# Performance work log

Measured on AMD Instinct MI355X. Metric: run time of the kernel, lower is better.

The kernel has to match this reference:

```python
import jax, jax.numpy as jnp
import numpy as np

HEADS = 8
DIM_HEAD = 64
KNN = 32
SCALE = DIM_HEAD ** -0.5


def setup_inputs() -> dict:
    key = jax.random.key(0)
    k1, k2, k3 = jax.random.split(key, 3)
    B, N, C = 2, 2048, 256
    inner = HEADS * DIM_HEAD  # 512
    x = jax.random.normal(k1, (B, N, C), dtype=jnp.float32)
    Wqkv = jax.random.normal(k2, (C, 3 * inner), dtype=jnp.float32) * (C ** -0.5)
    Wout = jax.random.normal(k3, (inner, C), dtype=jnp.float32) * (inner ** -0.5)
    bout = jnp.zeros((C,), dtype=jnp.float32)
    return {"x": x, "Wqkv": Wqkv, "Wout": Wout, "bout": bout}


def _knn_adjacency(x, k):
    # x: [B, N, C] -> boolean adjacency [B, N, N], k nearest neighbors by
    # euclidean distance, self-loops excluded (loop=False).
    B, N, _ = x.shape
    x2 = jnp.sum(x * x, axis=-1)  # [B, N]
    # squared distances [B, N, N]
    d2 = x2[:, :, None] + x2[:, None, :] - 2.0 * jnp.einsum('bnc,bmc->bnm', x, x)
    big = jnp.finfo(d2.dtype).max
    d2 = d2 + big * jnp.eye(N, dtype=d2.dtype)  # exclude self
    _, idx = jax.lax.top_k(-d2, k)  # [B, N, k] nearest neighbor indices

    rows = jnp.arange(N)[:, None]  # [N, 1]

    def scatter_one(idx_b):
        return jnp.zeros((N, N), dtype=bool).at[rows, idx_b].set(True)

    return jax.vmap(scatter_one)(idx)  # [B, N, N]


def reference(x, Wqkv, Wout, bout):
    B, N, C = x.shape
    adj = _knn_adjacency(x, KNN)  # [B, N, N] bool, shared across heads

    qkv = x @ Wqkv  # [B, N, 3*inner]
    q, k, v = jnp.split(qkv, 3, axis=-1)
    split_heads = lambda t: t.reshape(B, N, HEADS, DIM_HEAD).transpose(0, 2, 1, 3)
    q, k, v = split_heads(q), split_heads(k), split_heads(v)  # [B, H, N, d]

    dots = jnp.einsum('bhnd,bhmd->bhnm', q, k) * SCALE  # [B, H, N, N]
    dots = jnp.where(adj[:, None, :, :], dots, -jnp.inf)
    attn = jax.nn.softmax(dots, axis=-1)
    out = jnp.einsum('bhnm,bhmd->bhnd', attn, v)  # [B, H, N, d]
    out = out.transpose(0, 2, 1, 3).reshape(B, N, HEADS * DIM_HEAD)
    return out @ Wout + bout
```

## Files before the change

kernel.cpp:

```cpp
#include <hip/hip_runtime.h>
#include <hip/hip_bf16.h>
#include <hip/hip_fp16.h>

#define BATCH 2
#define NPTS  2048
#define CDIM  256
#define NHEAD 8
#define DHEAD 64
#define INNER 512
#define TRIPLE 1536
#define KNN   32
#define SCALE 0.125f

typedef __attribute__((ext_vector_type(8))) short short8;
typedef __attribute__((ext_vector_type(4))) float floatx4;
typedef __attribute__((ext_vector_type(4))) unsigned short ushort4v;
typedef unsigned short ushort;

#define TW  32
#define TSZ (128*TW)

__device__ __forceinline__ unsigned bfsplit(float x) {
    unsigned u = __float_as_uint(x);
    unsigned r = u + 0x7fffu + ((u >> 16) & 1u);
    unsigned hs = r >> 16;
    float hf = __uint_as_float(hs << 16);
    float lo = x - hf;
    unsigned u2 = __float_as_uint(lo);
    unsigned r2 = u2 + 0x7fffu + ((u2 >> 16) & 1u);
    return (hs & 0xffffu) | (r2 & 0xffff0000u);
}

__device__ __forceinline__ void bfsplit3(float x, ushort* hh, ushort* ll, ushort* qq) {
    unsigned u = __float_as_uint(x);
    unsigned r = u + 0x7fffu + ((u >> 16) & 1u);
    unsigned hs = r >> 16;
    float hf = __uint_as_float(hs << 16);
    float d1 = x - hf;
    unsigned u2 = __float_as_uint(d1);
    unsigned r2 = u2 + 0x7fffu + ((u2 >> 16) & 1u);
    unsigned ls = r2 >> 16;
    float lf = __uint_as_float(ls << 16);
    float d2 = d1 - lf;
    unsigned u3 = __float_as_uint(d2);
    unsigned r3 = u3 + 0x7fffu + ((u3 >> 16) & 1u);
    *hh = (ushort)hs;
    *ll = (ushort)ls;
    *qq = (ushort)(r3 >> 16);
}

__device__ __forceinline__ ushort f2h(float f) {
    __half h = __float2half(f);
    return *reinterpret_cast<ushort*>(&h);
}
__device__ __forceinline__ float h2f(ushort u) {
    __half h;
    *reinterpret_cast<ushort*>(&h) = u;
    return __half2float(h);
}

__global__ __launch_bounds__(256) void input_prep_kernel(const float* __restrict__ x,
                                                         float* __restrict__ x2,
                                                         ushort* __restrict__ xhi,
                                                         ushort* __restrict__ xlo,
                                                         ushort* __restrict__ xqd) {
    int wave = threadIdx.x >> 6, lane = threadIdx.x & 63;
    int row = blockIdx.x * 4 + wave;
    const float* xr = x + (size_t)row * CDIM;
    float4 v = *(const float4*)(xr + lane * 4);
    float s = v.x*v.x + v.y*v.y + v.z*v.z + v.w*v.w;
    #pragma unroll
    for (int o = 32; o; o >>= 1) s += __shfl_down(s, o);
    if (lane == 0) x2[row] = s;

    ushort h[4], l[4], q[4];
    bfsplit3(v.x, &h[0], &l[0], &q[0]);
    bfsplit3(v.y, &h[1], &l[1], &q[1]);
    bfsplit3(v.z, &h[2], &l[2], &q[2]);
    bfsplit3(v.w, &h[3], &l[3], &q[3]);
    size_t off = (size_t)row * CDIM + lane * 4;
    *(ushort4v*)(xhi + off) = *(ushort4v*)h;
    *(ushort4v*)(xlo + off) = *(ushort4v*)l;
    *(ushort4v*)(xqd + off) = *(ushort4v*)q;
}

__global__ __launch_bounds__(256) void wtrans2_kernel(const float* __restrict__ Wqkv,
                                                      const float* __restrict__ Wout,
                                                      ushort* __restrict__ wqhiT,
                                                      ushort* __restrict__ wqloT,
                                                      ushort* __restrict__ wohiT,
                                                      ushort* __restrict__ woloT) {
    __shared__ float tile[64][65];
    const float* W; ushort* hiT; ushort* loT; int K, N, bx, by;
    int bid = blockIdx.x;
    if (bid < 96) { W = Wqkv; hiT = wqhiT; loT = wqloT; K = CDIM;  N = TRIPLE; bx = bid % 24; by = bid / 24; }
    else { int t = bid - 96; W = Wout; hiT = wohiT; loT = woloT; K = INNER; N = CDIM;  bx = t % 4;  by = t / 4; }
    int k0 = by * 64, n0 = bx * 64;
    #pragma unroll
    for (int i = 0; i < 4; ++i) {
        int f = threadIdx.x + i * 256;
        int r = f >> 4, c4 = (f & 15) * 4;
        float4 v = *(const float4*)(W + (size_t)(k0 + r) * N + n0 + c4);
        tile[r][c4+0] = v.x; tile[r][c4+1] = v.y;
        tile[r][c4+2] = v.z; tile[r][c4+3] = v.w;
    }
    __syncthreads();
    #pragma unroll
    for (int i = 0; i < 4; ++i) {
        int f = threadIdx.x + i * 256;
        int rn = f >> 4, ck = (f & 15) * 4;
        unsigned p0 = bfsplit(tile[ck+0][rn]);
        unsigned p1 = bfsplit(tile[ck+1][rn]);
        unsigned p2 = bfsplit(tile[ck+2][rn]);
        unsigned p3 = bfsplit(tile[ck+3][rn]);
        ushort4v h, l;
        h.x = (ushort)p0; l.x = (ushort)(p0 >> 16);
        h.y = (ushort)p1; l.y = (ushort)(p1 >> 16);
        h.z = (ushort)p2; l.z = (ushort)(p2 >> 16);
        h.w = (ushort)p3; l.w = (ushort)(p3 >> 16);
        *(ushort4v*)(hiT + (size_t)(n0 + rn) * K + k0 + ck) = h;
        *(ushort4v*)(loT + (size_t)(n0 + rn) * K + k0 + ck) = l;
    }
}


__device__ __forceinline__ void gemm_split_body(const ushort* __restrict__ Ahi,
                                                const ushort* __restrict__ Alo,
                                                const ushort* __restrict__ BhiT,
                                                const ushort* __restrict__ BloT,
                                                const float* __restrict__ bias,
                                                float* __restrict__ C,
                                                int N, int K, int bi, int bj,
                                                ushort* lds,
                                                ushort* __restrict__ kv16) {
    int lane = threadIdx.x & 63, wave = threadIdx.x >> 6;
    int wr = wave >> 1, wc = wave & 1;
    int fr = lane & 15, kg = lane >> 4;
    int swz8 = (kg ^ ((fr >> 1) & 3)) * 8;

    int srow = threadIdx.x >> 1;
    int hc = (threadIdx.x & 1) * 2;
    int sw = (srow >> 1) & 3;
    int d0 = srow * TW + ((hc + 0) ^ sw) * 8;
    int d1 = srow * TW + ((hc + 1) ^ sw) * 8;

    const ushort* g0 = Ahi  + (size_t)(bi + srow) * K + hc * 8;
    const ushort* g1 = Alo  + (size_t)(bi + srow) * K + hc * 8;
    const ushort* g2 = BhiT + (size_t)(bj + srow) * K + hc * 8;
    const ushort* g3 = BloT + (size_t)(bj + srow) * K + hc * 8;

    floatx4 acc[4][4] = {};

    for (int k0 = 0; k0 < K; k0 += 32) {
        uint4 va0 = *(const uint4*)(g0 + k0);
        uint4 va1 = *(const uint4*)(g0 + k0 + 8);
        uint4 vb0 = *(const uint4*)(g1 + k0);
        uint4 vb1 = *(const uint4*)(g1 + k0 + 8);
        uint4 vc0 = *(const uint4*)(g2 + k0);
        uint4 vc1 = *(const uint4*)(g2 + k0 + 8);
        uint4 vd0 = *(const uint4*)(g3 + k0);
        uint4 vd1 = *(const uint4*)(g3 + k0 + 8);
        *(uint4*)&lds[0*TSZ + d0] = va0;  *(uint4*)&lds[0*TSZ + d1] = va1;
        *(uint4*)&lds[1*TSZ + d0] = vb0;  *(uint4*)&lds[1*TSZ + d1] = vb1;
        *(uint4*)&lds[2*TSZ + d0] = vc0;  *(uint4*)&lds[2*TSZ + d1] = vc1;
        *(uint4*)&lds[3*TSZ + d0] = vd0;  *(uint4*)&lds[3*TSZ + d1] = vd1;
        __syncthreads();

        short8 a_h[4], a_l[4], b_h[4], b_l[4];
        #pragma unroll
        for (int m = 0; m < 4; ++m) {
            int off = (wr*64 + m*16 + fr) * TW + swz8;
            a_h[m] = *(const short8*)&lds[0*TSZ + off];
            a_l[m] = *(const short8*)&lds[1*TSZ + off];
        }
        #pragma unroll
        for (int n = 0; n < 4; ++n) {
            int off = (wc*64 + n*16 + fr) * TW + swz8;
            b_h[n] = *(const short8*)&lds[2*TSZ + off];
            b_l[n] = *(const short8*)&lds[3*TSZ + off];
        }
        #pragma unroll
        for (int m = 0; m < 4; ++m)
            #pragma unroll
            for (int n = 0; n < 4; ++n) {
                acc[m][n] = __builtin_amdgcn_mfma_f32_16x16x32_bf16(a_h[m], b_h[n], acc[m][n], 0, 0, 0);
                acc[m][n] = __builtin_amdgcn_mfma_f32_16x16x32_bf16(a_h[m], b_l[n], acc[m][n], 0, 0, 0);
                acc[m][n] = __builtin_amdgcn_mfma_f32_16x16x32_bf16(a_l[m], b_h[n], acc[m][n], 0, 0, 0);
            }
        __syncthreads();
    }

    #pragma unroll
    for (int m = 0; m < 4; ++m)
        #pragma unroll
        for (int n = 0; n < 4; ++n) {
            int col = bj + wc*64 + n*16 + fr;
            float bv = bias ? bias[col] : 0.0f;
            #pragma unroll
            for (int r = 0; r < 4; ++r) {
                int row = bi + wr*64 + m*16 + kg*4 + r;
                float val = acc[m][n][r] + bv;
                C[(size_t)row * N + col] = val;
                if (kv16 && col >= INNER)
                    kv16[(size_t)row * 1024 + (col - INNER)] = f2h(val);
            }
        }
}

__device__ __forceinline__ void gram_body(const ushort* __restrict__ Ah,
                                          const ushort* __restrict__ Al,
                                          const ushort* __restrict__ Aq,
                                          const float* __restrict__ x2b,
                                          float* __restrict__ Sb,
                                          int bi, int bj, ushort* lds) {
    int lane = threadIdx.x & 63, wave = threadIdx.x >> 6;
    int wr = wave >> 1, wc = wave & 1;
    int fr = lane & 15, kg = lane >> 4;
    int swz8 = (kg ^ ((fr >> 1) & 3)) * 8;

    int srow = threadIdx.x >> 1;
    int hc = (threadIdx.x & 1) * 2;
    int sw = (srow >> 1) & 3;
    int d0 = srow * TW + ((hc + 0) ^ sw) * 8;
    int d1 = srow * TW + ((hc + 1) ^ sw) * 8;

    const ushort* g0 = Ah + (size_t)(bi + srow) * CDIM + hc * 8;
    const ushort* g1 = Al + (size_t)(bi + srow) * CDIM + hc * 8;
    const ushort* g2 = Aq + (size_t)(bi + srow) * CDIM + hc * 8;
    const ushort* g3 = Ah + (size_t)(bj + srow) * CDIM + hc * 8;
    const ushort* g4 = Al + (size_t)(bj + srow) * CDIM + hc * 8;
    const ushort* g5 = Aq + (size_t)(bj + srow) * CDIM + hc * 8;

    floatx4 acc[4][4] = {};

    for (int k0 = 0; k0 < CDIM; k0 += 32) {
        uint4 a0 = *(const uint4*)(g0 + k0); uint4 a1 = *(const uint4*)(g0 + k0 + 8);
        uint4 b0 = *(const uint4*)(g1 + k0); uint4 b1 = *(const uint4*)(g1 + k0 + 8);
        uint4 c0 = *(const uint4*)(g2 + k0); uint4 c1 = *(const uint4*)(g2 + k0 + 8);
        uint4 e0 = *(const uint4*)(g3 + k0); uint4 e1 = *(const uint4*)(g3 + k0 + 8);
        uint4 f0 = *(const uint4*)(g4 + k0); uint4 f1 = *(const uint4*)(g4 + k0 + 8);
        uint4 h0 = *(const uint4*)(g5 + k0); uint4 h1 = *(const uint4*)(g5 + k0 + 8);
        *(uint4*)&lds[0*TSZ + d0] = a0; *(uint4*)&lds[0*TSZ + d1] = a1;
        *(uint4*)&lds[1*TSZ + d0] = b0; *(uint4*)&lds[1*TSZ + d1] = b1;
        *(uint4*)&lds[2*TSZ + d0] = c0; *(uint4*)&lds[2*TSZ + d1] = c1;
        *(uint4*)&lds[3*TSZ + d0] = e0; *(uint4*)&lds[3*TSZ + d1] = e1;
        *(uint4*)&lds[4*TSZ + d0] = f0; *(uint4*)&lds[4*TSZ + d1] = f1;
        *(uint4*)&lds[5*TSZ + d0] = h0; *(uint4*)&lds[5*TSZ + d1] = h1;
        __syncthreads();

        short8 a_h[4], a_l[4], a_q[4], b_h[4], b_l[4], b_q[4];
        #pragma unroll
        for (int m = 0; m < 4; ++m) {
            int off = (wr*64 + m*16 + fr) * TW + swz8;
            a_h[m] = *(const short8*)&lds[0*TSZ + off];
            a_l[m] = *(const short8*)&lds[1*TSZ + off];
            a_q[m] = *(const short8*)&lds[2*TSZ + off];
        }
        #pragma unroll
        for (int n = 0; n < 4; ++n) {
            int off = (wc*64 + n*16 + fr) * TW + swz8;
            b_h[n] = *(const short8*)&lds[3*TSZ + off];
            b_l[n] = *(const short8*)&lds[4*TSZ + off];
            b_q[n] = *(const short8*)&lds[5*TSZ + off];
        }
        #pragma unroll
        for (int m = 0; m < 4; ++m)
            #pragma unroll
            for (int n = 0; n < 4; ++n) {
                acc[m][n] = __builtin_amdgcn_mfma_f32_16x16x32_bf16(a_h[m], b_h[n], acc[m][n], 0, 0, 0);
                acc[m][n] = __builtin_amdgcn_mfma_f32_16x16x32_bf16(a_h[m], b_l[n], acc[m][n], 0, 0, 0);
                acc[m][n] = __builtin_amdgcn_mfma_f32_16x16x32_bf16(a_l[m], b_h[n], acc[m][n], 0, 0, 0);
                acc[m][n] = __builtin_amdgcn_mfma_f32_16x16x32_bf16(a_l[m], b_l[n], acc[m][n], 0, 0, 0);
                acc[m][n] = __builtin_amdgcn_mfma_f32_16x16x32_bf16(a_h[m], b_q[n], acc[m][n], 0, 0, 0);
                acc[m][n] = __builtin_amdgcn_mfma_f32_16x16x32_bf16(a_q[m], b_h[n], acc[m][n], 0, 0, 0);
            }
        __syncthreads();
    }

    #pragma unroll
    for (int m = 0; m < 4; ++m)
        #pragma unroll
        for (int n = 0; n < 4; ++n) {
            int col = bj + wc*64 + n*16 + fr;
            float xc = x2b[col];
            #pragma unroll
            for (int r = 0; r < 4; ++r) {
                int row = bi + wr*64 + m*16 + kg*4 + r;
                float val = xc - 2.0f * acc[m][n][r];
                if (row == col) val = __builtin_inff();
                Sb[(size_t)row * NPTS + col] = val;
            }
        }

    if (bi != bj) {
        float* T = (float*)lds;
        #pragma unroll
        for (int p = 0; p < 2; ++p) {
            __syncthreads();
            if (wc == p) {
                #pragma unroll
                for (int m = 0; m < 4; ++m) {
                    int row0 = wr*64 + m*16 + kg*4;
                    float x0 = x2b[bi + row0 + 0];
                    float x1 = x2b[bi + row0 + 1];
                    float x2v = x2b[bi + row0 + 2];
                    float x3 = x2b[bi + row0 + 3];
                    #pragma unroll
                    for (int n = 0; n < 4; ++n) {
                        int colp = n*16 + fr;
                        float4 v;
                        v.x = x0 - 2.0f * acc[m][n][0];
                        v.y = x1 - 2.0f * acc[m][n][1];
                        v.z = x2v - 2.0f * acc[m][n][2];
                        v.w = x3 - 2.0f * acc[m][n][3];
                        *(float4*)&T[colp * 132 + row0] = v;
                    }
                }
            }
            __syncthreads();
            #pragma unroll
            for (int i = 0; i < 8; ++i) {
                int f = threadIdx.x + i * 256;
                int cr = f >> 5, c4 = (f & 31) * 4;
                float4 v = *(const float4*)&T[cr * 132 + c4];
                *(float4*)(Sb + (size_t)(bj + p*64 + cr) * NPTS + bi + c4) = v;
            }
        }
    }
}

__global__ __launch_bounds__(256) void fused_mfma_kernel(const ushort* __restrict__ xh,
                                                         const ushort* __restrict__ xl,
                                                         const ushort* __restrict__ xq,
                                                         const float* __restrict__ x2,
                                                         float* __restrict__ S,
                                                         const ushort* __restrict__ wqhiT,
                                                         const ushort* __restrict__ wqloT,
                                                         float* __restrict__ qkv,
                                                         ushort* __restrict__ kv16) {
    __shared__ ushort lds[6*TSZ];
    int bid = blockIdx.x;
    if (bid < 272) {
        int b = bid / 136, t = bid % 136;
        int by = 0;
        while (t >= 16 - by) { t -= 16 - by; ++by; }
        int bx = by + t;
        size_t xoff = (size_t)b * NPTS * CDIM;
        gram_body(xh + xoff, xl + xoff, xq + xoff,
                  x2 + (size_t)b * NPTS, S + (size_t)b * NPTS * NPTS,
                  by * 128, bx * 128, lds);
    } else {
        int t = bid - 272;
        int bx = t % 12, by = t / 12;
        gemm_split_body(xh, xl, wqhiT, wqloT, nullptr, qkv,
                        TRIPLE, CDIM, by * 128, bx * 128, lds, kv16);
    }
}

__global__ __launch_bounds__(256) void outproj_kernel(const ushort* __restrict__ Ahi,
                                                      const ushort* __restrict__ Alo,
                                                      const ushort* __restrict__ BhiT,
                                                      const ushort* __restrict__ BloT,
                                                      const float* __restrict__ bias,
                                                      float* __restrict__ C) {
    __shared__ ushort lds[4*TSZ];
    gemm_split_body(Ahi, Alo, BhiT, BloT, bias, C,
                    CDIM, INNER, blockIdx.y * 128, blockIdx.x * 128, lds, nullptr);
}

__device__ __forceinline__ unsigned block_excl_scan_256(unsigned c,
                                                        unsigned* wsum,
                                                        unsigned* total_out) {
    unsigned v = c;
    #pragma unroll
    for (int o = 1; o < 64; o <<= 1) {
        unsigned t = __shfl_up(v, o);
        if ((threadIdx.x & 63) >= o) v += t;
    }
    if ((threadIdx.x & 63) == 63) wsum[threadIdx.x >> 6] = v;
    __syncthreads();
    unsigned woff = 0;
    int mywave = threadIdx.x >> 6;
    #pragma unroll
    for (int w = 0; w < 4; ++w) {
        unsigned s = wsum[w];
        if (w < mywave) woff += s;
    }
    if (total_out) *total_out = wsum[0] + wsum[1] + wsum[2] + wsum[3];
    __syncthreads();
    return v + woff - c;
}

__global__ __launch_bounds__(256) void knn_attn_kernel(const float* __restrict__ S,
                                                       const float* __restrict__ qkv,
                                                       const ushort* __restrict__ kv16,
                                                       ushort* __restrict__ ahi,
                                                       ushort* __restrict__ alo) {
    int bid = blockIdx.x;
    int b = (bid & 7) >> 2;
    int n = ((bid >> 3) << 2) | (bid & 3);
    size_t rowoff = (size_t)b * NPTS + n;
    const float* row = S + rowoff * NPTS;

    __shared__ unsigned keys[NPTS];
    __shared__ unsigned hist[256];
    __shared__ unsigned wsum[4];
    __shared__ unsigned s_red[8];
    __shared__ unsigned sh_lo, sh_hi, sh_rank, sh_cnt, sh_break;
    __shared__ unsigned ckey[64];
    __shared__ int     cidx[64];
    __shared__ unsigned s_ccount;
    __shared__ int   nb[KNN];
    __shared__ float dots[NHEAD][KNN];
    __shared__ float p[NHEAD][KNN];

    int tid = threadIdx.x;

    unsigned mn = 0xffffffffu, mx = 0u;
    {
        int i0 = tid * 8;
        float4 f0 = *(const float4*)(row + i0);
        float4 f1 = *(const float4*)(row + i0 + 4);
        float fv[8] = { f0.x, f0.y, f0.z, f0.w, f1.x, f1.y, f1.z, f1.w };
        #pragma unroll
        for (int t = 0; t < 8; ++t) {
            int i = i0 + t;
            unsigned u;
            if (i == n) {
                u = 0xffffffffu;
            } else {
                unsigned v = __float_as_uint(fv[t]);
                u = (v & 0x80000000u) ? ~v : (v | 0x80000000u);
                mn = min(mn, u); mx = max(mx, u);
            }
            keys[i] = u;
        }
    }
    #pragma unroll
    for (int o = 32; o; o >>= 1) {
        mn = min(mn, (unsigned)__shfl_xor((int)mn, o));
        mx = max(mx, (unsigned)__shfl_xor((int)mx, o));
    }
    if ((tid & 63) == 0) { s_red[tid >> 6] = mn; s_red[4 + (tid >> 6)] = mx; }
    __syncthreads();
    if (tid == 0) {
        unsigned a = min(min(s_red[0], s_red[1]), min(s_red[2], s_red[3]));
        unsigned z = max(max(s_red[4], s_red[5]), max(s_red[6], s_red[7]));
        sh_lo = a; sh_hi = z; sh_rank = KNN; sh_break = 0; s_ccount = 0;
    }
    __syncthreads();

    for (int it = 0; it < 5; ++it) {
        unsigned lo = sh_lo, hi = sh_hi;
        unsigned range1 = hi - lo;
        int shift = 0;
        if (range1 > 255u) shift = 24 - __clz(range1);
        hist[tid] = 0;
        __syncthreads();
        for (int i = tid; i < NPTS; i += 256) {
            unsigned u = keys[i];
            if (u >= lo && u <= hi)
                atomicAdd(&hist[(u - lo) >> shift], 1u);
        }
        __syncthreads();
        unsigned c = hist[tid];
        unsigned rank = sh_rank;
        unsigned excl = block_excl_scan_256(c, wsum, nullptr);
        if (excl < rank && excl + c >= rank) {
            sh_rank = rank - excl;
            unsigned nlo = lo + ((unsigned)tid << shift);
            unsigned span = (shift == 0) ? 0u : (((1u << shift)) - 1u);
            unsigned nhi = nlo + span;
            if (nhi > hi || nhi < nlo) nhi = hi;
            sh_lo = nlo; sh_hi = nhi;
            sh_cnt = c;
            sh_break = (shift == 0 || c <= 64u) ? 1u : 0u;
        }
        __syncthreads();
        if (sh_break) break;
    }

    unsigned lo = sh_lo, hi = sh_hi, rank = sh_rank, cnt = sh_cnt;

    unsigned lt = 0;
    for (int i = tid; i < NPTS; i += 256) lt += (keys[i] < lo) ? 1u : 0u;
    unsigned pos = block_excl_scan_256(lt, wsum, nullptr);
    for (int i = tid; i < NPTS; i += 256) {
        unsigned u = keys[i];
        if (u < lo) nb[pos++] = i;
        else if (u >= lo && u <= hi && cnt <= 64u) {
            unsigned pp = atomicAdd(&s_ccount, 1u);
            ckey[pp] = u; cidx[pp] = i;
        }
    }
    __syncthreads();

    unsigned base = KNN - rank;
    if (cnt <= 64u) {
        if (tid < (int)cnt) {
            unsigned myk = ckey[tid]; int myi = cidx[tid];
            unsigned r = 0;
            for (unsigned s = 0; s < cnt; ++s) {
                unsigned sk = ckey[s]; int si = cidx[s];
                r += (sk < myk || (sk == myk && si < myi)) ? 1u : 0u;
            }
            if (r < rank) nb[base + r] = myi;
        }
    } else {
        if (tid == 0) {
            unsigned need = rank, pp = base;
            for (int i = 0; i < NPTS && need; ++i) {
                if (keys[i] >= lo && keys[i] <= hi) { nb[pp++] = i; --need; }
            }
        }
    }
    __syncthreads();

    const float* qrow = qkv + rowoff * TRIPLE;
    const ushort* kvb = kv16 + (size_t)b * NPTS * 1024;

    {
        int j = tid >> 3;
        int l = tid & 7;
        const ushort* krow = kvb + (size_t)nb[j] * 1024 + l * 8;
        short8 kr[NHEAD];
        #pragma unroll
        for (int h = 0; h < NHEAD; ++h)
            kr[h] = *(const short8*)(krow + h * DHEAD);
        const float* qp = qrow + l * 8;
        #pragma unroll
        for (int h = 0; h < NHEAD; ++h) {
            float4 q0 = *(const float4*)(qp + h * DHEAD);
            float4 q1 = *(const float4*)(qp + h * DHEAD + 4);
            float d = h2f((ushort)kr[h][0]) * q0.x + h2f((ushort)kr[h][1]) * q0.y
                    + h2f((ushort)kr[h][2]) * q0.z + h2f((ushort)kr[h][3]) * q0.w
                    + h2f((ushort)kr[h][4]) * q1.x + h2f((ushort)kr[h][5]) * q1.y
                    + h2f((ushort)kr[h][6]) * q1.z + h2f((ushort)kr[h][7]) * q1.w;
            d += __shfl_xor(d, 1);
            d += __shfl_xor(d, 2);
            d += __shfl_xor(d, 4);
            if (l == 0) dots[h][j] = d * SCALE;
        }
    }
    __syncthreads();

    {
        int h = tid >> 5, jj = tid & 31;
        float dv = dots[h][jj];
        float mxv = dv;
        for (int o = 16; o; o >>= 1) mxv = fmaxf(mxv, __shfl_xor(mxv, o));
        float e = expf(dv - mxv);
        float s = e;
        for (int o = 16; o; o >>= 1) s += __shfl_xor(s, o);
        p[h][jj] = e / s;
    }
    __syncthreads();

    {
        int hd = tid >> 5;
        int jd = tid & 31;
        const ushort* vb = kvb + INNER + hd * DHEAD + jd * 2;
        float o0 = 0.f, o1 = 0.f;
        #pragma unroll
        for (int g = 0; g < 4; ++g) {
            unsigned vv[8]; float pw[8];
            #pragma unroll
            for (int t = 0; t < 8; ++t) {
                int jj = g * 8 + t;
                vv[t] = *(const unsigned*)(vb + (size_t)nb[jj] * 1024);
                pw[t] = p[hd][jj];
            }
            #pragma unroll
            for (int t = 0; t < 8; ++t) {
                o0 += pw[t] * h2f((ushort)(vv[t] & 0xffffu));
                o1 += pw[t] * h2f((ushort)(vv[t] >> 16));
            }
        }
        size_t baseo = rowoff * INNER + hd * DHEAD + jd * 2;
        unsigned q0 = bfsplit(o0);
        unsigned q1 = bfsplit(o1);
        *(unsigned*)(ahi + baseo) = (q0 & 0xffffu) | (q1 << 16);
        *(unsigned*)(alo + baseo) = (q0 >> 16) | (q1 & 0xffff0000u);
    }
}

extern "C" void kernel_launch(void* const* d_in, const int* in_sizes, int n_in,
                              void* d_out, int out_size, void* d_ws, size_t ws_size,
                              hipStream_t stream) {
    const float* x    = (const float*)d_in[0];
    const float* Wqkv = (const float*)d_in[1];
    const float* Wout = (const float*)d_in[2];
    const float* bout = (const float*)d_in[3];
    float* out = (float*)d_out;

    float* S    = (float*)d_ws;
    float* x2   = S + (size_t)BATCH * NPTS * NPTS;
    float* qkv  = x2 + (size_t)BATCH * NPTS;
    ushort* kv16 = (ushort*)(qkv + (size_t)BATCH * NPTS * TRIPLE);
    ushort* xhi = kv16 + (size_t)BATCH * NPTS * 1024;
    ushort* xlo   = xhi   + (size_t)BATCH * NPTS * CDIM;
    ushort* xqd   = xlo   + (size_t)BATCH * NPTS * CDIM;
    ushort* ahi   = xqd   + (size_t)BATCH * NPTS * CDIM;
    ushort* alo   = ahi   + (size_t)BATCH * NPTS * INNER;
    ushort* wqhiT = alo   + (size_t)BATCH * NPTS * INNER;
    ushort* wqloT = wqhiT + (size_t)TRIPLE * CDIM;
    ushort* wohiT = wqloT + (size_t)TRIPLE * CDIM;
    ushort* woloT = wohiT + (size_t)CDIM * INNER;

    input_prep_kernel<<<(BATCH * NPTS) / 4, 256, 0, stream>>>(x, x2, xhi, xlo, xqd);

    wtrans2_kernel<<<128, 256, 0, stream>>>(Wqkv, Wout, wqhiT, wqloT, wohiT, woloT);

    fused_mfma_kernel<<<656, 256, 0, stream>>>(xhi, xlo, xqd, x2, S,
                                               wqhiT, wqloT, qkv, kv16);

    knn_attn_kernel<<<BATCH * NPTS, 256, 0, stream>>>(S, qkv, kv16, ahi, alo);

    {
        dim3 grid(CDIM / 128, (BATCH * NPTS) / 128);
        outproj_kernel<<<grid, 256, 0, stream>>>(ahi, alo, wohiT, woloT, bout, out);
    }
}
```

Before: 109.0 us.

## Use atomic work queue in fused GEMM kernel and drop redundant fp32 K/V stores

Replaces the static block-to-tile mapping in the fused Gram/QKV kernel with a persistent-style loop: blocks pull items from a global atomic counter that the input-prep kernel resets. Gram tiles are handed out first and QKV tiles after, which is meant to improve load balance. The QKV epilogue now writes only Q in fp32, into a compact [rows,512] buffer, and K/V only as fp16. This removes the redundant fp32 K/V stores and their memory traffic. The cost is an atomic plus two block barriers per item, and a 768-block grid that oversubscribes the 656 items.

```diff
diff --git a/kernel.cpp b/kernel.cpp
--- a/kernel.cpp
+++ b/kernel.cpp
@@ -11,6 +11,10 @@
 #define TRIPLE 1536
 #define KNN   32
 #define SCALE 0.125f
+
+#define GRAM_ITEMS 272
+#define QKV_ITEMS  384
+#define TOTAL_ITEMS (GRAM_ITEMS + QKV_ITEMS)
 
 typedef __attribute__((ext_vector_type(8))) short short8;
 typedef __attribute__((ext_vector_type(4))) float floatx4;
@@ -63,7 +67,9 @@
                                                          float* __restrict__ x2,
                                                          ushort* __restrict__ xhi,
                                                          ushort* __restrict__ xlo,
-                                                         ushort* __restrict__ xqd) {
+                                                         ushort* __restrict__ xqd,
+                                                         unsigned* __restrict__ wq) {
+    if (blockIdx.x == 0 && threadIdx.x == 0) *wq = 0u;
     int wave = threadIdx.x >> 6, lane = threadIdx.x & 63;
     int row = blockIdx.x * 4 + wave;
     const float* xr = x + (size_t)row * CDIM;
@@ -190,21 +196,35 @@
         __syncthreads();
     }
 
-    #pragma unroll
-    for (int m = 0; m < 4; ++m)
-        #pragma unroll
-        for (int n = 0; n < 4; ++n) {
-            int col = bj + wc*64 + n*16 + fr;
-            float bv = bias ? bias[col] : 0.0f;
-            #pragma unroll
-            for (int r = 0; r < 4; ++r) {
-                int row = bi + wr*64 + m*16 + kg*4 + r;
-                float val = acc[m][n][r] + bv;
-                C[(size_t)row * N + col] = val;
-                if (kv16 && col >= INNER)
-                    kv16[(size_t)row * 1024 + (col - INNER)] = f2h(val);
-            }
-        }
+    if (kv16) {
+        bool is_q = (bj < INNER);
+        #pragma unroll
+        for (int m = 0; m < 4; ++m)
+            #pragma unroll
+            for (int n = 0; n < 4; ++n) {
+                int col = bj + wc*64 + n*16 + fr;
+                #pragma unroll
+                for (int r = 0; r < 4; ++r) {
+                    int row = bi + wr*64 + m*16 + kg*4 + r;
+                    float val = acc[m][n][r];
+                    if (is_q) C[(size_t)row * INNER + col] = val;
+                    else      kv16[(size_t)row * 1024 + (col - INNER)] = f2h(val);
+                }
+            }
+    } else {
+        #pragma unroll
+        for (int m = 0; m < 4; ++m)
+            #pragma unroll
+            for (int n = 0; n < 4; ++n) {
+                int col = bj + wc*64 + n*16 + fr;
+                float bv = bias ? bias[col] : 0.0f;
+                #pragma unroll
+                for (int r = 0; r < 4; ++r) {
+                    int row = bi + wr*64 + m*16 + kg*4 + r;
+                    C[(size_t)row * N + col] = acc[m][n][r] + bv;
+                }
+            }
+    }
 }
 
 __device__ __forceinline__ void gram_body(const ushort* __restrict__ Ah,
@@ -336,24 +356,32 @@
                                                          float* __restrict__ S,
                                                          const ushort* __restrict__ wqhiT,
                                                          const ushort* __restrict__ wqloT,
-                                                         float* __restrict__ qkv,
-                                                         ushort* __restrict__ kv16) {
+                                                         float* __restrict__ q,
+                                                         ushort* __restrict__ kv16,
+                                                         unsigned* __restrict__ wq) {
     __shared__ ushort lds[6*TSZ];
-    int bid = blockIdx.x;
-    if (bid < 272) {
-        int b = bid / 136, t = bid % 136;
-        int by = 0;
-        while (t >= 16 - by) { t -= 16 - by; ++by; }
-        int bx = by + t;
-        size_t xoff = (size_t)b * NPTS * CDIM;
-        gram_body(xh + xoff, xl + xoff, xq + xoff,
-                  x2 + (size_t)b * NPTS, S + (size_t)b * NPTS * NPTS,
-                  by * 128, bx * 128, lds);
-    } else {
-        int t = bid - 272;
-        int bx = t % 12, by = t / 12;
-        gemm_split_body(xh, xl, wqhiT, wqloT, nullptr, qkv,
-                        TRIPLE, CDIM, by * 128, bx * 128, lds, kv16);
+    __shared__ int s_item;
+    while (true) {
+        __syncthreads();
+        if (threadIdx.x == 0) s_item = (int)atomicAdd(wq, 1u);
+        __syncthreads();
+        int item = s_item;
+        if (item >= TOTAL_ITEMS) break;
+        if (item < GRAM_ITEMS) {
+            int b = item / 136, t = item % 136;
+            int by = 0;
+            while (t >= 16 - by) { t -= 16 - by; ++by; }
+            int bx = by + t;
+            size_t xoff = (size_t)b * NPTS * CDIM;
+            gram_body(xh + xoff, xl + xoff, xq + xoff,
+                      x2 + (size_t)b * NPTS, S + (size_t)b * NPTS * NPTS,
+                      by * 128, bx * 128, lds);
+        } else {
+            int t = item - GRAM_ITEMS;
+            int bx = t % 12, by = t / 12;
+            gemm_split_body(xh, xl, wqhiT, wqloT, nullptr, q,
+                            TRIPLE, CDIM, by * 128, bx * 128, lds, kv16);
+        }
     }
 }
 
@@ -392,7 +420,7 @@
 }
 
 __global__ __launch_bounds__(256) void knn_attn_kernel(const float* __restrict__ S,
-                                                       const float* __restrict__ qkv,
+                                                       const float* __restrict__ q,
                                                        const ushort* __restrict__ kv16,
                                                        ushort* __restrict__ ahi,
                                                        ushort* __restrict__ alo) {
@@ -516,7 +544,7 @@
     }
     __syncthreads();
 
-    const float* qrow = qkv + rowoff * TRIPLE;
+    const float* qrow = q + rowoff * INNER;
     const ushort* kvb = kv16 + (size_t)b * NPTS * 1024;
 
     {
@@ -593,11 +621,11 @@
     const float* bout = (const float*)d_in[3];
     float* out = (float*)d_out;
 
-    float* S    = (float*)d_ws;
-    float* x2   = S + (size_t)BATCH * NPTS * NPTS;
-    float* qkv  = x2 + (size_t)BATCH * NPTS;
-    ushort* kv16 = (ushort*)(qkv + (size_t)BATCH * NPTS * TRIPLE);
-    ushort* xhi = kv16 + (size_t)BATCH * NPTS * 1024;
+    float* S     = (float*)d_ws;
+    float* x2    = S + (size_t)BATCH * NPTS * NPTS;
+    float* q     = x2 + (size_t)BATCH * NPTS;
+    ushort* kv16 = (ushort*)(q + (size_t)BATCH * NPTS * INNER);
+    ushort* xhi  = kv16 + (size_t)BATCH * NPTS * 1024;
     ushort* xlo   = xhi   + (size_t)BATCH * NPTS * CDIM;
     ushort* xqd   = xlo   + (size_t)BATCH * NPTS * CDIM;
     ushort* ahi   = xqd   + (size_t)BATCH * NPTS * CDIM;
@@ -606,15 +634,16 @@
     ushort* wqloT = wqhiT + (size_t)TRIPLE * CDIM;
     ushort* wohiT = wqloT + (size_t)TRIPLE * CDIM;
     ushort* woloT = wohiT + (size_t)CDIM * INNER;
-
-    input_prep_kernel<<<(BATCH * NPTS) / 4, 256, 0, stream>>>(x, x2, xhi, xlo, xqd);
+    unsigned* wq  = (unsigned*)(woloT + (size_t)CDIM * INNER);
+
+    input_prep_kernel<<<(BATCH * NPTS) / 4, 256, 0, stream>>>(x, x2, xhi, xlo, xqd, wq);
 
     wtrans2_kernel<<<128, 256, 0, stream>>>(Wqkv, Wout, wqhiT, wqloT, wohiT, woloT);
 
-    fused_mfma_kernel<<<656, 256, 0, stream>>>(xhi, xlo, xqd, x2, S,
-                                               wqhiT, wqloT, qkv, kv16);
-
-    knn_attn_kernel<<<BATCH * NPTS, 256, 0, stream>>>(S, qkv, kv16, ahi, alo);
+    fused_mfma_kernel<<<768, 256, 0, stream>>>(xhi, xlo, xqd, x2, S,
+                                               wqhiT, wqloT, q, kv16, wq);
+
+    knn_attn_kernel<<<BATCH * NPTS, 256, 0, stream>>>(S, q, kv16, ahi, alo);
 
     {
         dim3 grid(CDIM / 128, (BATCH * NPTS) / 128);
```

Measured after the change: 114.0 us. +4.6%, slower.
